# Optimization experiments

Measured on AMD Instinct MI355X. Metric: run time of the kernel, lower is better.

The kernel has to match this reference:

```python
import jax, jax.numpy as jnp
import numpy as np

MUL = 32            # multiplicity of each irrep
N_NODES = 16384
N_EDGES = 262144
AVG_NEIGH = 16.0
N_SPECIES = 4
RADIAL_DIM = 8
INV_SQRT3 = 0.5773502691896258  # normalized CG coeff for 1o x 1o -> 0e (dot)


def setup_inputs() -> dict:
    key = jax.random.key(0)
    ks = jax.random.split(key, 14)
    f32 = jnp.float32
    return {
        "node_features": jax.random.normal(ks[0], (N_NODES, 4 * MUL), dtype=f32),
        "edge_sh": jax.random.normal(ks[1], (N_EDGES, 4), dtype=f32),
        "radial_embedding": jax.random.uniform(ks[2], (N_EDGES, RADIAL_DIM), dtype=f32),
        "W_up_s": jax.random.normal(ks[3], (MUL, MUL), dtype=f32),
        "W_up_v": jax.random.normal(ks[4], (MUL, MUL), dtype=f32),
        "W_r1": jax.random.normal(ks[5], (RADIAL_DIM, RADIAL_DIM), dtype=f32),
        "W_r2": jax.random.normal(ks[6], (RADIAL_DIM, 4 * MUL), dtype=f32),
        "W_dn_s": jax.random.normal(ks[7], (2 * MUL, 2 * MUL), dtype=f32),
        "W_dn_v": jax.random.normal(ks[8], (2 * MUL, MUL), dtype=f32),
        "W_sk_s": jax.random.normal(ks[9], (N_SPECIES, MUL, 2 * MUL), dtype=f32),
        "W_sk_v": jax.random.normal(ks[10], (N_SPECIES, MUL, MUL), dtype=f32),
        "senders": jax.random.randint(ks[11], (N_EDGES,), 0, N_NODES),
        "receivers": jax.random.randint(ks[12], (N_EDGES,), 0, N_NODES),
        "node_species": jax.random.randint(ks[13], (N_NODES,), 0, N_SPECIES),
    }


def reference(node_features, edge_sh, radial_embedding, W_up_s, W_up_v,
              W_r1, W_r2, W_dn_s, W_dn_v, W_sk_s, W_sk_v,
              senders, receivers, node_species):
    n = node_features.shape[0]
    # irreps layout: 32x0e (first MUL cols) + 32x1o (next 3*MUL cols)
    s = node_features[:, :MUL]                      # [N, mul]     0e
    v = node_features[:, MUL:].reshape(n, MUL, 3)   # [N, mul, 3]  1o

    # linear_up: per-irrep channel mixing, 1/sqrt(fan_in) normalization
    s1 = (s @ W_up_s) * (MUL ** -0.5)
    v1 = jnp.einsum('nmi,mk->nki', v, W_up_v) * (MUL ** -0.5)

    # gather sender features per edge
    ss = s1[senders]              # [E, mul]
    vs = v1[senders]              # [E, mul, 3]
    yv = edge_sh[:, 1:4]          # 1o part of edge spherical harmonics (0e part dropped in TP)

    # Clebsch-Gordan tensor product, filtered to output irreps {0e, 1o}:
    #   0e x 1o -> 1o ;  1o x 1o -> 0e (dot, coeff 1/sqrt(3)); cross(1e) & 2e dropped
    m_v_tp = ss[:, :, None] * yv[:, None, :]                 # [E, mul, 3]
    m_s_tp = jnp.einsum('emi,ei->em', vs, yv) * INV_SQRT3    # [E, mul]

    # radial MLP -> one scalar weight per irrep instance of the message
    h = jax.nn.silu((radial_embedding @ W_r1) * (RADIAL_DIM ** -0.5))
    w = (h @ W_r2) * (RADIAL_DIM ** -0.5)                    # [E, 4*mul]
    w_ss, w_vs, w_vt, w_st = jnp.split(w, 4, axis=1)

    # message = concat(self-features, tensor-product paths), radially weighted
    m_s = jnp.concatenate([ss * w_ss, m_s_tp * w_st], axis=1)                          # [E, 2*mul]
    m_v = jnp.concatenate([vs * w_vs[:, :, None], m_v_tp * w_vt[:, :, None]], axis=1)  # [E, 2*mul, 3]

    # scatter-add into receiver nodes, divide by sqrt(avg_num_neighbours)
    inv = AVG_NEIGH ** -0.5
    S = jax.ops.segment_sum(m_s, receivers, num_segments=n) * inv                     # [N, 2*mul]
    V = jax.ops.segment_sum(m_v.reshape(m_v.shape[0], -1), receivers,
                            num_segments=n).reshape(n, 2 * MUL, 3) * inv              # [N, 2*mul, 3]

    # linear_down to gate irreps: MUL 0e features + MUL gate scalars, MUL 1o vectors
    g_s = (S @ W_dn_s) * ((2 * MUL) ** -0.5)                                          # [N, 2*mul]
    g_v = jnp.einsum('nmi,mk->nki', V, W_dn_v) * ((2 * MUL) ** -0.5)                  # [N, mul, 3]

    # species-indexed skip connection from the original node features
    sk_s = jnp.einsum('nm,nmk->nk', s, W_sk_s[node_species]) * (MUL ** -0.5)
    sk_v = jnp.einsum('nmi,nmk->nki', v, W_sk_v[node_species]) * (MUL ** -0.5)
    g_s = 0.5 * (g_s + sk_s)
    g_v = 0.5 * (g_v + sk_v)

    # gate nonlinearity: silu on even scalars, silu(gates) multiplies each 1o vector
    feat_s = jax.nn.silu(g_s[:, :MUL])
    gates = jax.nn.silu(g_s[:, MUL:])
    out_v = g_v * gates[:, :, None]
    return jnp.concatenate([feat_s, out_v.reshape(n, 3 * MUL)], axis=1)  # [N, 4*mul]
```

## Files before the change

### kernel.cpp

```cpp
#include <hip/hip_runtime.h>
#include <hip/hip_bf16.h>
#include <hip/hip_fp16.h>

#define N_NODES 16384
#define N_EDGES 262144
#define MUL 32

__device__ __forceinline__ float silu_f(float x) {
    return x / (1.0f + __expf(-x));
}
__device__ __forceinline__ __half2 i2h2(int v) { return __builtin_bit_cast(__half2, v); }
__device__ __forceinline__ int h22i(__half2 v) { return __builtin_bit_cast(int, v); }

__global__ void k_up(const float* __restrict__ nf,
                     const float* __restrict__ Wus,
                     const float* __restrict__ Wuv,
                     __half* __restrict__ up_h,
                     const int* __restrict__ recv,
                     int* __restrict__ counts) {
    __shared__ float sh[2][128];
    int node0 = blockIdx.x * 2;
    int t = threadIdx.x;
    if (t < 32) {
        int e = blockIdx.x * 32 + t;
        atomicAdd(&counts[recv[e]], 1);
    }
    sh[t >> 7][t & 127] = nf[(size_t)node0 * 128 + t];
    __syncthreads();
    int local = t >> 7;
    int c = t & 127;
    int m = c >> 2, comp = c & 3;
    const float* row = sh[local];
    float acc = 0.f;
    if (comp == 0) {
        #pragma unroll
        for (int k = 0; k < 32; ++k) acc += row[k] * Wus[k * 32 + m];
    } else {
        int i = comp - 1;
        #pragma unroll
        for (int k = 0; k < 32; ++k) acc += row[32 + k * 3 + i] * Wuv[k * 32 + m];
    }
    up_h[(size_t)(node0 + local) * 128 + c] = __float2half(acc * 0.17677669529663687f);
}

__global__ void k_scan(const int* __restrict__ counts,
                       int* __restrict__ starts,
                       int* __restrict__ cursor) {
    __shared__ int wtot[16];
    __shared__ int woff[16];
    int t = threadIdx.x;
    int lane = t & 63, wid = t >> 6;
    const int4* cp = (const int4*)(counts + t * 16);
    int4 c0 = cp[0], c1 = cp[1], c2 = cp[2], c3 = cp[3];
    int cs[16] = {c0.x,c0.y,c0.z,c0.w,c1.x,c1.y,c1.z,c1.w,
                  c2.x,c2.y,c2.z,c2.w,c3.x,c3.y,c3.z,c3.w};
    int mysum = 0;
    #pragma unroll
    for (int i = 0; i < 16; ++i) mysum += cs[i];
    int incl = mysum;
    #pragma unroll
    for (int off = 1; off < 64; off <<= 1) {
        int y = __shfl_up(incl, off, 64);
        if (lane >= off) incl += y;
    }
    if (lane == 63) wtot[wid] = incl;
    __syncthreads();
    if (t == 0) {
        int run = 0;
        #pragma unroll
        for (int w = 0; w < 16; ++w) { woff[w] = run; run += wtot[w]; }
    }
    __syncthreads();
    int run = woff[wid] + (incl - mysum);
    #pragma unroll
    for (int i = 0; i < 16; ++i) {
        starts[t * 16 + i] = run;
        cursor[t * 16 + i] = run;
        run += cs[i];
    }
    if (t == 1023) starts[N_NODES] = run;
}

__global__ void k_edges(const float* __restrict__ rad,
                        const float* __restrict__ Wr1,
                        const int* __restrict__ recv,
                        const int* __restrict__ senders,
                        const float* __restrict__ esh,
                        int* __restrict__ cursor,
                        int4* __restrict__ records) {
    int e = blockIdx.x * blockDim.x + threadIdx.x;
    const float4* rp = (const float4*)(rad + (size_t)e * 8);
    float4 a = rp[0], b = rp[1];
    float r[8] = {a.x, a.y, a.z, a.w, b.x, b.y, b.z, b.w};
    float h[8];
    #pragma unroll
    for (int j = 0; j < 8; ++j) {
        float acc = 0.f;
        #pragma unroll
        for (int k = 0; k < 8; ++k) acc += r[k] * Wr1[k * 8 + j];
        h[j] = silu_f(acc * 0.35355339059327373f);
    }
    float4 ey = *(const float4*)(esh + (size_t)e * 4);
    int snd = senders[e];
    int rc = recv[e];
    int pos = atomicAdd(&cursor[rc], 1);
    int4 meta;
    meta.x = snd;
    meta.y = h22i(__floats2half2_rn(ey.y, ey.z));
    meta.z = h22i(__floats2half2_rn(ey.w, 0.f));
    meta.w = 0;
    int4 hp;
    hp.x = h22i(__floats2half2_rn(h[0], h[1]));
    hp.y = h22i(__floats2half2_rn(h[2], h[3]));
    hp.z = h22i(__floats2half2_rn(h[4], h[5]));
    hp.w = h22i(__floats2half2_rn(h[6], h[7]));
    records[2 * (size_t)pos] = meta;
    records[2 * (size_t)pos + 1] = hp;
}

struct Acc {
    float S0, S1, Vv0, Vv1, Vv2, Vt0, Vt1, Vt2;
};
__device__ __forceinline__ void edge_accum(int4 meta, int4 hp, int2 q,
                                           const float* __restrict__ wr2a,
                                           const float* __restrict__ wr2b,
                                           const float* __restrict__ wr2c,
                                           const float* __restrict__ wr2d,
                                           Acc& A) {
    float2 h01 = __half22float2(i2h2(hp.x));
    float2 h23 = __half22float2(i2h2(hp.y));
    float2 h45 = __half22float2(i2h2(hp.z));
    float2 h67 = __half22float2(i2h2(hp.w));
    float h[8] = {h01.x, h01.y, h23.x, h23.y, h45.x, h45.y, h67.x, h67.y};
    float wss = 0.f, wvs = 0.f, wvt = 0.f, wst = 0.f;
    #pragma unroll
    for (int j = 0; j < 8; ++j) {
        wss += h[j] * wr2a[j];
        wvs += h[j] * wr2b[j];
        wvt += h[j] * wr2c[j];
        wst += h[j] * wr2d[j];
    }
    float2 y01 = __half22float2(i2h2(meta.y));
    float2 y2p = __half22float2(i2h2(meta.z));
    float y0 = y01.x, y1 = y01.y, y2 = y2p.x;
    float2 sv0 = __half22float2(i2h2(q.x));
    float2 v12 = __half22float2(i2h2(q.y));
    float ss = sv0.x, v0 = sv0.y, v1v = v12.x, v2 = v12.y;
    float dot = v0 * y0 + v1v * y1 + v2 * y2;
    A.S0 += ss * wss;
    A.S1 += dot * wst;
    A.Vv0 += v0 * wvs; A.Vv1 += v1v * wvs; A.Vv2 += v2 * wvs;
    float tv = ss * wvt;
    A.Vt0 += tv * y0; A.Vt1 += tv * y1; A.Vt2 += tv * y2;
}

__launch_bounds__(256, 4)
__global__ void k_gather(const __half* __restrict__ up_h,
                         const float* __restrict__ nf,
                         const int4* __restrict__ records,
                         const float* __restrict__ Wr2,
                         const int* __restrict__ starts,
                         const float* __restrict__ Wdns,
                         const float* __restrict__ Wdnv,
                         const float* __restrict__ Wsks,
                         const float* __restrict__ Wskv,
                         const int* __restrict__ species,
                         float* __restrict__ out) {
    __shared__ float agg[4][256];
    __shared__ float snode[4][32];
    __shared__ float vnode[4][96];

    int tid = threadIdx.x;
    int w = tid >> 6;
    int lane = tid & 63;
    int sub = lane >> 5;
    int m = lane & 31;
    int node = blockIdx.x * 4 + w;

    int s0 = starts[node], s1 = starts[node + 1];

    int ta = s0 + sub, tb = s0 + 2 + sub;
    bool va = ta < s1, vb = tb < s1;
    int4 ra0 = make_int4(0,0,0,0), ra1 = ra0, rb0 = ra0, rb1 = ra0;
    if (va) { const int4* p = records + 2 * (size_t)ta; ra0 = p[0]; ra1 = p[1]; }
    if (vb) { const int4* p = records + 2 * (size_t)tb; rb0 = p[0]; rb1 = p[1]; }

    {
        const float* src = nf + (size_t)node * 128;
        #pragma unroll
        for (int it = 0; it < 2; ++it) {
            int c = lane + it * 64;
            float v = src[c];
            if (c < 32) snode[w][c] = v;
            else        vnode[w][c - 32] = v;
        }
    }

    const float s8 = 0.35355339059327373f;
    const float s8s3 = 0.35355339059327373f * 0.5773502691896258f;
    float wr2a[8], wr2b[8], wr2c[8], wr2d[8];
    #pragma unroll
    for (int j = 0; j < 8; ++j) {
        wr2a[j] = Wr2[j * 128 + m] * s8;
        wr2b[j] = Wr2[j * 128 + 32 + m] * s8;
        wr2c[j] = Wr2[j * 128 + 64 + m] * s8;
        wr2d[j] = Wr2[j * 128 + 96 + m] * s8s3;
    }

    Acc A = {0.f,0.f,0.f,0.f,0.f,0.f,0.f,0.f};
    Acc B = {0.f,0.f,0.f,0.f,0.f,0.f,0.f,0.f};

    for (int t0 = s0; t0 < s1; t0 += 4) {
        int2 qa = make_int2(0,0), qb = qa;
        if (va) qa = *(const int2*)(up_h + (size_t)ra0.x * 128 + m * 4);
        if (vb) qb = *(const int2*)(up_h + (size_t)rb0.x * 128 + m * 4);

        int tn = t0 + 4;
        int nta = tn + sub, ntb = tn + 2 + sub;
        bool nva = nta < s1, nvb = ntb < s1;
        int4 na0 = make_int4(0,0,0,0), na1 = na0, nb0 = na0, nb1 = na0;
        if (nva) { const int4* p = records + 2 * (size_t)nta; na0 = p[0]; na1 = p[1]; }
        if (nvb) { const int4* p = records + 2 * (size_t)ntb; nb0 = p[0]; nb1 = p[1]; }

        if (va) edge_accum(ra0, ra1, qa, wr2a, wr2b, wr2c, wr2d, A);
        if (vb) edge_accum(rb0, rb1, qb, wr2a, wr2b, wr2c, wr2d, B);

        ra0 = na0; ra1 = na1; rb0 = nb0; rb1 = nb1;
        va = nva; vb = nvb;
    }

    float accS0 = A.S0 + B.S0, accS1 = A.S1 + B.S1;
    float accVv0 = A.Vv0 + B.Vv0, accVv1 = A.Vv1 + B.Vv1, accVv2 = A.Vv2 + B.Vv2;
    float accVt0 = A.Vt0 + B.Vt0, accVt1 = A.Vt1 + B.Vt1, accVt2 = A.Vt2 + B.Vt2;

    accS0 += __shfl_xor(accS0, 32, 64);
    accS1 += __shfl_xor(accS1, 32, 64);
    accVv0 += __shfl_xor(accVv0, 32, 64);
    accVv1 += __shfl_xor(accVv1, 32, 64);
    accVv2 += __shfl_xor(accVv2, 32, 64);
    accVt0 += __shfl_xor(accVt0, 32, 64);
    accVt1 += __shfl_xor(accVt1, 32, 64);
    accVt2 += __shfl_xor(accVt2, 32, 64);

    const float inv_neigh = 0.25f;
    if (sub == 0) {
        agg[w][m]               = accS0 * inv_neigh;
        agg[w][32 + m]          = accS1 * inv_neigh;
        agg[w][64 + 3 * m + 0]  = accVv0 * inv_neigh;
        agg[w][64 + 3 * m + 1]  = accVv1 * inv_neigh;
        agg[w][64 + 3 * m + 2]  = accVv2 * inv_neigh;
        agg[w][160 + 3 * m + 0] = accVt0 * inv_neigh;
        agg[w][160 + 3 * m + 1] = accVt1 * inv_neigh;
        agg[w][160 + 3 * m + 2] = accVt2 * inv_neigh;
    }

    const float* S = agg[w];
    const float* V = agg[w] + 64;
    int sp = species[node];

    float gsa = 0.f, gsb = 0.f, gv0 = 0.f, gv1 = 0.f, gv2 = 0.f;
    {
        int mm0 = sub * 32;
        #pragma unroll 4
        for (int k = 0; k < 32; ++k) {
            int mm = mm0 + k;
            float Sm = S[mm];
            gsa += Sm * Wdns[mm * 64 + m];
            gsb += Sm * Wdns[mm * 64 + 32 + m];
            float wv = Wdnv[mm * 32 + m];
            gv0 += V[mm * 3 + 0] * wv;
            gv1 += V[mm * 3 + 1] * wv;
            gv2 += V[mm * 3 + 2] * wv;
        }
    }
    float ska = 0.f, skb = 0.f, skv0 = 0.f, skv1 = 0.f, skv2 = 0.f;
    {
        const float* Ws = Wsks + (size_t)sp * 2048;
        const float* Wv = Wskv + (size_t)sp * 1024;
        int mm0 = sub * 16;
        #pragma unroll 4
        for (int k = 0; k < 16; ++k) {
            int mm = mm0 + k;
            float sm = snode[w][mm];
            ska += sm * Ws[mm * 64 + m];
            skb += sm * Ws[mm * 64 + 32 + m];
            float wv = Wv[mm * 32 + m];
            skv0 += vnode[w][mm * 3 + 0] * wv;
            skv1 += vnode[w][mm * 3 + 1] * wv;
            skv2 += vnode[w][mm * 3 + 2] * wv;
        }
    }
    gsa += __shfl_xor(gsa, 32, 64);
    gsb += __shfl_xor(gsb, 32, 64);
    gv0 += __shfl_xor(gv0, 32, 64);
    gv1 += __shfl_xor(gv1, 32, 64);
    gv2 += __shfl_xor(gv2, 32, 64);
    ska += __shfl_xor(ska, 32, 64);
    skb += __shfl_xor(skb, 32, 64);
    skv0 += __shfl_xor(skv0, 32, 64);
    skv1 += __shfl_xor(skv1, 32, 64);
    skv2 += __shfl_xor(skv2, 32, 64);

    if (sub == 0) {
        const float inv8 = 0.125f;
        const float isq32 = 0.17677669529663687f;
        float a  = 0.5f * (gsa * inv8 + ska * isq32);
        float b  = 0.5f * (gsb * inv8 + skb * isq32);
        float o0 = 0.5f * (gv0 * inv8 + skv0 * isq32);
        float o1 = 0.5f * (gv1 * inv8 + skv1 * isq32);
        float o2 = 0.5f * (gv2 * inv8 + skv2 * isq32);

        float feat = silu_f(a);
        float gate = silu_f(b);
        float* o = out + (size_t)node * 128;
        o[m] = feat;
        o[32 + 3 * m + 0] = o0 * gate;
        o[32 + 3 * m + 1] = o1 * gate;
        o[32 + 3 * m + 2] = o2 * gate;
    }
}

extern "C" void kernel_launch(void* const* d_in, const int* in_sizes, int n_in,
                              void* d_out, int out_size, void* d_ws, size_t ws_size,
                              hipStream_t stream) {
    const float* nf   = (const float*)d_in[0];
    const float* esh  = (const float*)d_in[1];
    const float* rad  = (const float*)d_in[2];
    const float* Wus  = (const float*)d_in[3];
    const float* Wuv  = (const float*)d_in[4];
    const float* Wr1  = (const float*)d_in[5];
    const float* Wr2  = (const float*)d_in[6];
    const float* Wdns = (const float*)d_in[7];
    const float* Wdnv = (const float*)d_in[8];
    const float* Wsks = (const float*)d_in[9];
    const float* Wskv = (const float*)d_in[10];
    const int* senders   = (const int*)d_in[11];
    const int* receivers = (const int*)d_in[12];
    const int* species   = (const int*)d_in[13];
    float* out = (float*)d_out;

    char* ws = (char*)d_ws;
    __half* up_h   = (__half*)(ws);
    int4* records  = (int4*)(ws + (4u << 20));
    int* counts    = (int*)(ws + (12u << 20));
    int* cursor    = (int*)(ws + (12u << 20) + 65536);
    int* starts    = (int*)(ws + (12u << 20) + 131072);

    hipMemsetAsync(counts, 0, 65536, stream);
    k_up<<<N_NODES / 2, 256, 0, stream>>>(nf, Wus, Wuv, up_h, receivers, counts);
    k_scan<<<1, 1024, 0, stream>>>(counts, starts, cursor);
    k_edges<<<N_EDGES / 256, 256, 0, stream>>>(rad, Wr1, receivers, senders, esh,
                                               cursor, records);
    k_gather<<<N_NODES / 4, 256, 0, stream>>>(up_h, nf, records, Wr2, starts,
                                              Wdns, Wdnv, Wsks, Wskv, species, out);
}
```

Baseline: 185.1 us.

## Reuse counting-pass atomic ranks for edge placement and deepen gather prefetch

The counting pass now stores each edge's atomic return value as its rank within the receiver bucket. The edge kernel then places records at starts[recv]+rank instead of doing a second atomic on a cursor array, which also removes the cursor writes from the scan. Separately, the gather loop is turned into a two-stage software pipeline: the sender feature load for the next edge pair and the records two iterations ahead are issued before accumulating the current pair. This costs an extra 1 MB rank buffer plus its write and read, and raises register pressure in the gather kernel.

```diff
diff --git a/kernel.cpp b/kernel.cpp
--- a/kernel.cpp
+++ b/kernel.cpp
@@ -17,13 +17,14 @@
                      const float* __restrict__ Wuv,
                      __half* __restrict__ up_h,
                      const int* __restrict__ recv,
-                     int* __restrict__ counts) {
+                     int* __restrict__ counts,
+                     int* __restrict__ rank) {
     __shared__ float sh[2][128];
     int node0 = blockIdx.x * 2;
     int t = threadIdx.x;
     if (t < 32) {
         int e = blockIdx.x * 32 + t;
-        atomicAdd(&counts[recv[e]], 1);
+        rank[e] = atomicAdd(&counts[recv[e]], 1);
     }
     sh[t >> 7][t & 127] = nf[(size_t)node0 * 128 + t];
     __syncthreads();
@@ -44,8 +45,7 @@
 }
 
 __global__ void k_scan(const int* __restrict__ counts,
-                       int* __restrict__ starts,
-                       int* __restrict__ cursor) {
+                       int* __restrict__ starts) {
     __shared__ int wtot[16];
     __shared__ int woff[16];
     int t = threadIdx.x;
@@ -75,7 +75,6 @@
     #pragma unroll
     for (int i = 0; i < 16; ++i) {
         starts[t * 16 + i] = run;
-        cursor[t * 16 + i] = run;
         run += cs[i];
     }
     if (t == 1023) starts[N_NODES] = run;
@@ -86,7 +85,8 @@
                         const int* __restrict__ recv,
                         const int* __restrict__ senders,
                         const float* __restrict__ esh,
-                        int* __restrict__ cursor,
+                        const int* __restrict__ starts,
+                        const int* __restrict__ rank,
                         int4* __restrict__ records) {
     int e = blockIdx.x * blockDim.x + threadIdx.x;
     const float4* rp = (const float4*)(rad + (size_t)e * 8);
@@ -103,7 +103,7 @@
     float4 ey = *(const float4*)(esh + (size_t)e * 4);
     int snd = senders[e];
     int rc = recv[e];
-    int pos = atomicAdd(&cursor[rc], 1);
+    int pos = starts[rc] + rank[e];
     int4 meta;
     meta.x = snd;
     meta.y = h22i(__floats2half2_rn(ey.y, ey.z));
@@ -179,11 +179,14 @@
 
     int s0 = starts[node], s1 = starts[node + 1];
 
+    const int4 zi4 = make_int4(0,0,0,0);
+    const int2 zi2 = make_int2(0,0);
+
     int ta = s0 + sub, tb = s0 + 2 + sub;
-    bool va = ta < s1, vb = tb < s1;
-    int4 ra0 = make_int4(0,0,0,0), ra1 = ra0, rb0 = ra0, rb1 = ra0;
-    if (va) { const int4* p = records + 2 * (size_t)ta; ra0 = p[0]; ra1 = p[1]; }
-    if (vb) { const int4* p = records + 2 * (size_t)tb; rb0 = p[0]; rb1 = p[1]; }
+    bool vca = ta < s1, vcb = tb < s1;
+    int4 c0 = zi4, c1 = zi4, d0 = zi4, d1 = zi4;
+    if (vca) { const int4* p = records + 2 * (size_t)ta; c0 = p[0]; c1 = p[1]; }
+    if (vcb) { const int4* p = records + 2 * (size_t)tb; d0 = p[0]; d1 = p[1]; }
 
     {
         const float* src = nf + (size_t)node * 128;
@@ -196,6 +199,15 @@
         }
     }
 
+    int2 qa = zi2, qb = zi2;
+    if (vca) qa = *(const int2*)(up_h + (size_t)c0.x * 128 + m * 4);
+    if (vcb) qb = *(const int2*)(up_h + (size_t)d0.x * 128 + m * 4);
+
+    bool vna = ta + 4 < s1, vnb = tb + 4 < s1;
+    int4 n0 = zi4, n1 = zi4, e0 = zi4, e1 = zi4;
+    if (vna) { const int4* p = records + 2 * (size_t)(ta + 4); n0 = p[0]; n1 = p[1]; }
+    if (vnb) { const int4* p = records + 2 * (size_t)(tb + 4); e0 = p[0]; e1 = p[1]; }
+
     const float s8 = 0.35355339059327373f;
     const float s8s3 = 0.35355339059327373f * 0.5773502691896258f;
     float wr2a[8], wr2b[8], wr2c[8], wr2d[8];
@@ -211,22 +223,23 @@
     Acc B = {0.f,0.f,0.f,0.f,0.f,0.f,0.f,0.f};
 
     for (int t0 = s0; t0 < s1; t0 += 4) {
-        int2 qa = make_int2(0,0), qb = qa;
-        if (va) qa = *(const int2*)(up_h + (size_t)ra0.x * 128 + m * 4);
-        if (vb) qb = *(const int2*)(up_h + (size_t)rb0.x * 128 + m * 4);
-
-        int tn = t0 + 4;
-        int nta = tn + sub, ntb = tn + 2 + sub;
-        bool nva = nta < s1, nvb = ntb < s1;
-        int4 na0 = make_int4(0,0,0,0), na1 = na0, nb0 = na0, nb1 = na0;
-        if (nva) { const int4* p = records + 2 * (size_t)nta; na0 = p[0]; na1 = p[1]; }
-        if (nvb) { const int4* p = records + 2 * (size_t)ntb; nb0 = p[0]; nb1 = p[1]; }
-
-        if (va) edge_accum(ra0, ra1, qa, wr2a, wr2b, wr2c, wr2d, A);
-        if (vb) edge_accum(rb0, rb1, qb, wr2a, wr2b, wr2c, wr2d, B);
-
-        ra0 = na0; ra1 = na1; rb0 = nb0; rb1 = nb1;
-        va = nva; vb = nvb;
+        int2 qna = zi2, qnb = zi2;
+        if (vna) qna = *(const int2*)(up_h + (size_t)n0.x * 128 + m * 4);
+        if (vnb) qnb = *(const int2*)(up_h + (size_t)e0.x * 128 + m * 4);
+
+        int t2a = t0 + 8 + sub, t2b = t0 + 10 + sub;
+        bool v2a = t2a < s1, v2b = t2b < s1;
+        int4 p0 = zi4, p1 = zi4, r0 = zi4, r1 = zi4;
+        if (v2a) { const int4* p = records + 2 * (size_t)t2a; p0 = p[0]; p1 = p[1]; }
+        if (v2b) { const int4* p = records + 2 * (size_t)t2b; r0 = p[0]; r1 = p[1]; }
+
+        if (vca) edge_accum(c0, c1, qa, wr2a, wr2b, wr2c, wr2d, A);
+        if (vcb) edge_accum(d0, d1, qb, wr2a, wr2b, wr2c, wr2d, B);
+
+        c0 = n0; c1 = n1; d0 = e0; d1 = e1;
+        qa = qna; qb = qnb;
+        n0 = p0; n1 = p1; e0 = r0; e1 = r1;
+        vca = vna; vcb = vnb; vna = v2a; vnb = v2b;
     }
 
     float accS0 = A.S0 + B.S0, accS1 = A.S1 + B.S1;
@@ -343,14 +356,14 @@
     __half* up_h   = (__half*)(ws);
     int4* records  = (int4*)(ws + (4u << 20));
     int* counts    = (int*)(ws + (12u << 20));
-    int* cursor    = (int*)(ws + (12u << 20) + 65536);
-    int* starts    = (int*)(ws + (12u << 20) + 131072);
+    int* starts    = (int*)(ws + (12u << 20) + 65536);
+    int* rank      = (int*)(ws + (13u << 20));
 
     hipMemsetAsync(counts, 0, 65536, stream);
-    k_up<<<N_NODES / 2, 256, 0, stream>>>(nf, Wus, Wuv, up_h, receivers, counts);
-    k_scan<<<1, 1024, 0, stream>>>(counts, starts, cursor);
+    k_up<<<N_NODES / 2, 256, 0, stream>>>(nf, Wus, Wuv, up_h, receivers, counts, rank);
+    k_scan<<<1, 1024, 0, stream>>>(counts, starts);
     k_edges<<<N_EDGES / 256, 256, 0, stream>>>(rad, Wr1, receivers, senders, esh,
-                                               cursor, records);
+                                               starts, rank, records);
     k_gather<<<N_NODES / 4, 256, 0, stream>>>(up_h, nf, records, Wr2, starts,
                                               Wdns, Wdnv, Wsks, Wskv, species, out);
 }
```

Result: faster. 177.8 us (-3.9%).
